# Kernel tuning notes

Hardware: AMD Instinct MI355X
Metric: run time of the kernel (lower is better)

Reference implementation:

```python
import jax, jax.numpy as jnp
import numpy as np

N = 50000      # nodes
E = 500000     # edges
D_IN = 64      # node_in_dim
K = 4          # edge_in_dim
H = 64         # node_hidden_dim
C = 40         # num_class
L = 2          # num_layers


def setup_inputs() -> dict:
    key = jax.random.key(0)
    ks = jax.random.split(key, 10)
    node_features = jax.random.normal(ks[0], (N, D_IN), jnp.float32)
    edge_features = jax.random.normal(ks[1], (L, E, K), jnp.float32)
    src = jax.random.randint(ks[2], (E,), 0, N)
    dst = jax.random.randint(ks[3], (E,), 0, N)
    W0 = jax.random.normal(ks[4], (K * D_IN, H), jnp.float32) * 0.05
    b0 = jnp.zeros((H,), jnp.float32)
    W1 = jax.random.normal(ks[5], (K * H, H), jnp.float32) * 0.05
    b1 = jnp.zeros((H,), jnp.float32)
    Wfc = jax.random.normal(ks[6], (H, C), jnp.float32) * 0.05
    bfc = jnp.zeros((C,), jnp.float32)
    return dict(node_features=node_features, edge_features=edge_features,
                src=src, dst=dst, W0=W0, b0=b0, W1=W1, b1=b1, Wfc=Wfc, bfc=bfc)


def reference(node_features, edge_features, src, dst, W0, b0, W1, b1, Wfc, bfc):
    h = node_features  # [N, d]
    ones = jnp.ones((E,), jnp.float32)
    cnt = jnp.maximum(jax.ops.segment_sum(ones, dst, num_segments=N), 1.0)  # in-degree
    for i, (W, b) in enumerate([(W0, b0), (W1, b1)]):
        e = edge_features[i]          # [E, K]
        hs = h[src]                   # [E, d] edge gather of src node features
        d = hs.shape[1]
        # message: relu(Linear(flatten(e[:,:,None] * h[:,None,:])))
        # flatten order is (K, d), so reshape W -> [K, d, H] and contract directly
        Wr = W.reshape(K, d, H)
        m = jax.nn.relu(jnp.einsum('ek,ed,kdh->eh', e, hs, Wr) + b)  # [E, H]
        s = jax.ops.segment_sum(m, dst, num_segments=N)              # scatter-sum
        h = jax.nn.relu(s / cnt[:, None])                            # mailbox mean + relu
    return h @ Wfc + bfc  # [N, C]
```

## Files before the change

### kernel.cpp

```cpp
#include <hip/hip_runtime.h>
#include <hip/hip_fp16.h>

#define N_NODES 50000
#define N_EDGES 500000
#define DIM 64
#define KDIM 4
#define HID 64
#define NCLS 40
#define NBLK ((N_NODES + 255) / 256)
#define EBLK ((N_EDGES + 255) / 256)

__device__ inline unsigned pack2(float a, float b) {
    __half2 h = __floats2half2_rn(a, b);
    return *(unsigned*)&h;
}
__device__ inline float2 unpack2(unsigned u) {
    __half2 h = *(__half2*)&u;
    return __half22float2(h);
}

__global__ void hist_k(const int* __restrict__ dst, int* __restrict__ cnt) {
    int e = blockIdx.x * 256 + threadIdx.x;
    if (e < N_EDGES) atomicAdd(&cnt[dst[e]], 1);
}

__global__ __launch_bounds__(256) void scan_k(const int* __restrict__ cnt,
                                              int* __restrict__ start,
                                              int* __restrict__ cursor,
                                              volatile int* __restrict__ bflag,
                                              volatile int* __restrict__ bval) {
    __shared__ int ls[256];
    __shared__ int sbase;
    __shared__ int ok_all;
    int b = blockIdx.x, t = threadIdx.x;
    int n = b * 256 + t;
    int v = (n < N_NODES) ? cnt[n] : 0;
    ls[t] = v;
    __syncthreads();
#pragma unroll
    for (int off = 1; off < 256; off <<= 1) {
        int u = (t >= off) ? ls[t - off] : 0;
        __syncthreads();
        ls[t] += u;
        __syncthreads();
    }
    int incl = ls[t];
    int total = ls[255];
    __syncthreads();

    if (t == 0) {
        bval[b] = total;
        __threadfence();
        bflag[b] = 1;
    }

    if (b > 0) {
        for (;;) {
            int f = (t < b) ? bflag[t] : 1;
            if (t == 0) ok_all = 1;
            __syncthreads();
            if (!f) ok_all = 0;
            __syncthreads();
            if (ok_all) break;
        }
        __threadfence();
        int pv = (t < b) ? bval[t] : 0;
        ls[t] = pv;
        __syncthreads();
#pragma unroll
        for (int off = 128; off > 0; off >>= 1) {
            if (t < off) ls[t] += ls[t + off];
            __syncthreads();
        }
        if (t == 0) sbase = ls[0];
        __syncthreads();
    } else {
        if (t == 0) sbase = 0;
        __syncthreads();
    }

    int excl = sbase + incl - v;
    if (n < N_NODES) { start[n] = excl; cursor[n] = excl; }
    if (n == 0) start[N_NODES] = N_EDGES;
}

__global__ void scatter_k(const int* __restrict__ src, const int* __restrict__ dst,
                          const float* __restrict__ ef, int* __restrict__ cursor,
                          uint4* __restrict__ recA) {
    int e = blockIdx.x * 256 + threadIdx.x;
    if (e < N_EDGES) {
        int d = dst[e];
        int pos = atomicAdd(&cursor[d], 1);
        int sn = src[e];
        float4 f0 = ((const float4*)ef)[e];
        recA[pos] = make_uint4((unsigned)sn, pack2(f0.x, f0.y), pack2(f0.z, f0.w), (unsigned)e);
    }
}

__global__ void repack_k(const uint4* __restrict__ recA, const float* __restrict__ ef1,
                         uint4* __restrict__ recB) {
    int i = blockIdx.x * 256 + threadIdx.x;
    if (i < N_EDGES) {
        uint4 r = recA[i];
        int e = (int)r.w;
        float4 f1 = ((const float4*)ef1)[e];
        recB[i] = make_uint4(r.x, pack2(f1.x, f1.y), pack2(f1.z, f1.w), 0u);
    }
}

__global__ __launch_bounds__(256) void transform_k(const float* __restrict__ hin,
                                                   const float* __restrict__ W,
                                                   unsigned* __restrict__ y) {
    __shared__ float sW[2 * 64 * 64];
    __shared__ float sh[64 * 65];
    int t = threadIdx.x;
    int kpair = blockIdx.y;

    const float4* W4 = (const float4*)(W + (size_t)kpair * 2 * 4096);
    float4* sW4 = (float4*)sW;
#pragma unroll
    for (int i = 0; i < 8; ++i) sW4[t + 256 * i] = W4[t + 256 * i];

    int n0 = blockIdx.x * 64;
#pragma unroll
    for (int i = 0; i < 4; ++i) {
        int idx = t + 256 * i;
        int nl = idx >> 4;
        int dg = idx & 15;
        int n = n0 + nl;
        float4 v = make_float4(0.f, 0.f, 0.f, 0.f);
        if (n < N_NODES) v = ((const float4*)hin)[(size_t)n * 16 + dg];
        sh[nl * 65 + dg * 4 + 0] = v.x;
        sh[nl * 65 + dg * 4 + 1] = v.y;
        sh[nl * 65 + dg * 4 + 2] = v.z;
        sh[nl * 65 + dg * 4 + 3] = v.w;
    }
    __syncthreads();

    int nl = t & 31;
    int cg = t >> 5;
    int k_local = cg >> 2;
    int hc0 = (cg & 3) * 16;

    float acc0[16], acc1[16];
#pragma unroll
    for (int j = 0; j < 16; ++j) { acc0[j] = 0.f; acc1[j] = 0.f; }

    for (int d = 0; d < 64; ++d) {
        float a0 = sh[nl * 65 + d];
        float a1 = sh[(nl + 32) * 65 + d];
        const float* wr = &sW[k_local * 4096 + d * 64 + hc0];
#pragma unroll
        for (int j = 0; j < 16; ++j) {
            float w = wr[j];
            acc0[j] = fmaf(a0, w, acc0[j]);
            acc1[j] = fmaf(a1, w, acc1[j]);
        }
    }

    int n_a = n0 + nl, n_b = n0 + nl + 32;
    int cbase = (kpair * 2 + k_local) * 64 + hc0;
    if (n_a < N_NODES) {
        uint4* o = (uint4*)(y + ((size_t)n_a * 256 + cbase) / 2);
        o[0] = make_uint4(pack2(acc0[0], acc0[1]), pack2(acc0[2], acc0[3]),
                          pack2(acc0[4], acc0[5]), pack2(acc0[6], acc0[7]));
        o[1] = make_uint4(pack2(acc0[8], acc0[9]), pack2(acc0[10], acc0[11]),
                          pack2(acc0[12], acc0[13]), pack2(acc0[14], acc0[15]));
    }
    if (n_b < N_NODES) {
        uint4* o = (uint4*)(y + ((size_t)n_b * 256 + cbase) / 2);
        o[0] = make_uint4(pack2(acc1[0], acc1[1]), pack2(acc1[2], acc1[3]),
                          pack2(acc1[4], acc1[5]), pack2(acc1[6], acc1[7]));
        o[1] = make_uint4(pack2(acc1[8], acc1[9]), pack2(acc1[10], acc1[11]),
                          pack2(acc1[12], acc1[13]), pack2(acc1[14], acc1[15]));
    }
}

__device__ inline void load_edge(const uint4 r, const unsigned* __restrict__ y,
                                 int lane, uint2& q0, uint2& q1, uint2& q2, uint2& q3) {
    int sn = (int)r.x;
    const uint2* yb = (const uint2*)(y + (size_t)sn * 128);
    q0 = yb[lane];
    q1 = yb[16 + lane];
    q2 = yb[32 + lane];
    q3 = yb[48 + lane];
}

__device__ inline void compute_edge(const uint4 r, uint2 q0, uint2 q1, uint2 q2, uint2 q3,
                                    const float4 bias, float4& acc) {
    float2 e01 = unpack2(r.y);
    float2 e23 = unpack2(r.z);
    float2 a0 = unpack2(q0.x), a1 = unpack2(q0.y);
    float2 b0 = unpack2(q1.x), b1 = unpack2(q1.y);
    float2 c0 = unpack2(q2.x), c1 = unpack2(q2.y);
    float2 d0 = unpack2(q3.x), d1 = unpack2(q3.y);

    float4 z = bias;
    z.x = fmaf(e01.x, a0.x, z.x); z.y = fmaf(e01.x, a0.y, z.y);
    z.z = fmaf(e01.x, a1.x, z.z); z.w = fmaf(e01.x, a1.y, z.w);
    z.x = fmaf(e01.y, b0.x, z.x); z.y = fmaf(e01.y, b0.y, z.y);
    z.z = fmaf(e01.y, b1.x, z.z); z.w = fmaf(e01.y, b1.y, z.w);
    z.x = fmaf(e23.x, c0.x, z.x); z.y = fmaf(e23.x, c0.y, z.y);
    z.z = fmaf(e23.x, c1.x, z.z); z.w = fmaf(e23.x, c1.y, z.w);
    z.x = fmaf(e23.y, d0.x, z.x); z.y = fmaf(e23.y, d0.y, z.y);
    z.z = fmaf(e23.y, d1.x, z.z); z.w = fmaf(e23.y, d1.y, z.w);

    acc.x += fmaxf(z.x, 0.f);
    acc.y += fmaxf(z.y, 0.f);
    acc.z += fmaxf(z.z, 0.f);
    acc.w += fmaxf(z.w, 0.f);
}

__device__ inline float4 agg_core(const uint4* __restrict__ rec,
                                  const int* __restrict__ start,
                                  const int* __restrict__ cnt,
                                  const unsigned* __restrict__ y,
                                  const float* __restrict__ b,
                                  int g, int lane) {
    int s0 = start[g];
    int deg = cnt[g];
    int s1 = s0 + deg;

    float4 bias = ((const float4*)b)[lane];
    float4 acc = make_float4(0.f, 0.f, 0.f, 0.f);

    int i = s0;
    for (; i + 4 <= s1; i += 4) {
        uint4 r0 = rec[i + 0];
        uint4 r1 = rec[i + 1];
        uint4 r2 = rec[i + 2];
        uint4 r3 = rec[i + 3];
        uint2 a0, a1, a2, a3, b0, b1, b2, b3, c0, c1, c2, c3, d0, d1, d2, d3;
        load_edge(r0, y, lane, a0, a1, a2, a3);
        load_edge(r1, y, lane, b0, b1, b2, b3);
        load_edge(r2, y, lane, c0, c1, c2, c3);
        load_edge(r3, y, lane, d0, d1, d2, d3);
        compute_edge(r0, a0, a1, a2, a3, bias, acc);
        compute_edge(r1, b0, b1, b2, b3, bias, acc);
        compute_edge(r2, c0, c1, c2, c3, bias, acc);
        compute_edge(r3, d0, d1, d2, d3, bias, acc);
    }
    if (i + 2 <= s1) {
        uint4 r0 = rec[i + 0];
        uint4 r1 = rec[i + 1];
        uint2 a0, a1, a2, a3, b0, b1, b2, b3;
        load_edge(r0, y, lane, a0, a1, a2, a3);
        load_edge(r1, y, lane, b0, b1, b2, b3);
        compute_edge(r0, a0, a1, a2, a3, bias, acc);
        compute_edge(r1, b0, b1, b2, b3, bias, acc);
        i += 2;
    }
    if (i < s1) {
        uint4 r0 = rec[i];
        uint2 a0, a1, a2, a3;
        load_edge(r0, y, lane, a0, a1, a2, a3);
        compute_edge(r0, a0, a1, a2, a3, bias, acc);
    }

    float inv = 1.0f / (float)(deg > 1 ? deg : 1);
    float4 r;
    r.x = fmaxf(acc.x * inv, 0.f);
    r.y = fmaxf(acc.y * inv, 0.f);
    r.z = fmaxf(acc.z * inv, 0.f);
    r.w = fmaxf(acc.w * inv, 0.f);
    return r;
}

__global__ __launch_bounds__(256) void agg_k(const uint4* __restrict__ rec,
                                             const int* __restrict__ start,
                                             const int* __restrict__ cnt,
                                             const unsigned* __restrict__ y,
                                             const float* __restrict__ b,
                                             float* __restrict__ hout) {
    int t = blockIdx.x * 256 + threadIdx.x;
    int g = t >> 4;
    int lane = t & 15;
    float4 r = agg_core(rec, start, cnt, y, b, g, lane);
    ((float4*)hout)[(size_t)g * 16 + lane] = r;
}

__global__ __launch_bounds__(256) void agg_fc_k(const uint4* __restrict__ rec,
                                                const int* __restrict__ start,
                                                const int* __restrict__ cnt,
                                                const unsigned* __restrict__ y,
                                                const float* __restrict__ b,
                                                const float* __restrict__ Wfc,
                                                const float* __restrict__ bfc,
                                                float* __restrict__ out) {
    __shared__ float sh_h[16 * 65];
    __shared__ float sWfcT[NCLS * 65];
    __shared__ float sbfc[NCLS];
    int t = threadIdx.x;

    for (int i = t; i < 64 * NCLS; i += 256) {
        int j = i / NCLS;
        int c = i - j * NCLS;
        sWfcT[c * 65 + j] = Wfc[i];
    }
    if (t < NCLS) sbfc[t] = bfc[t];

    int nl = t >> 4;
    int lane = t & 15;
    int g = blockIdx.x * 16 + nl;

    float4 r = agg_core(rec, start, cnt, y, b, g, lane);
    sh_h[nl * 65 + lane * 4 + 0] = r.x;
    sh_h[nl * 65 + lane * 4 + 1] = r.y;
    sh_h[nl * 65 + lane * 4 + 2] = r.z;
    sh_h[nl * 65 + lane * 4 + 3] = r.w;
    __syncthreads();

    for (int item = t; item < 16 * NCLS; item += 256) {
        int rn = item / NCLS;
        int c = item - rn * NCLS;
        float acc = sbfc[c];
        const float* hr = &sh_h[rn * 65];
        const float* wc = &sWfcT[c * 65];
#pragma unroll
        for (int j = 0; j < 64; ++j) acc = fmaf(hr[j], wc[j], acc);
        out[(size_t)(blockIdx.x * 16 + rn) * NCLS + c] = acc;
    }
}

extern "C" void kernel_launch(void* const* d_in, const int* in_sizes, int n_in,
                              void* d_out, int out_size, void* d_ws, size_t ws_size,
                              hipStream_t stream) {
    const float* nf  = (const float*)d_in[0];
    const float* ef  = (const float*)d_in[1];
    const int*   src = (const int*)d_in[2];
    const int*   dst = (const int*)d_in[3];
    const float* W0  = (const float*)d_in[4];
    const float* b0  = (const float*)d_in[5];
    const float* W1  = (const float*)d_in[6];
    const float* b1  = (const float*)d_in[7];
    const float* Wfc = (const float*)d_in[8];
    const float* bfc = (const float*)d_in[9];
    float* out = (float*)d_out;

    char* ws = (char*)d_ws;
    size_t off = 0;
    auto alloc = [&](size_t bytes) -> void* {
        void* p = ws + off;
        off = (off + bytes + 255) & ~(size_t)255;
        return p;
    };
    int*      zbuf   = (int*)     alloc((size_t)(50176 + 512) * 4);
    int*      cnt    = zbuf;
    int*      bflag  = zbuf + 50176;
    int*      bval   = zbuf + 50176 + 256;
    int*      start  = (int*)     alloc((size_t)(N_NODES + 1) * 4);
    int*      cursor = (int*)     alloc((size_t)N_NODES * 4);
    uint4*    recA   = (uint4*)   alloc((size_t)N_EDGES * 16);
    uint4*    recB   = (uint4*)   alloc((size_t)N_EDGES * 16);
    unsigned* y      = (unsigned*)alloc((size_t)N_NODES * 256 * 2);
    float*    hbuf   = (float*)   alloc((size_t)N_NODES * 64 * 4);

    hipMemsetAsync(zbuf, 0, (size_t)(50176 + 512) * 4, stream);

    hist_k<<<EBLK, 256, 0, stream>>>(dst, cnt);
    scan_k<<<NBLK, 256, 0, stream>>>(cnt, start, cursor, bflag, bval);
    scatter_k<<<EBLK, 256, 0, stream>>>(src, dst, ef, cursor, recA);
    repack_k<<<EBLK, 256, 0, stream>>>(recA, ef + (size_t)N_EDGES * 4, recB);

    dim3 tgrid((N_NODES + 63) / 64, 2);
    int agrid = N_NODES / 16;

    transform_k<<<tgrid, 256, 0, stream>>>(nf, W0, y);
    agg_k<<<agrid, 256, 0, stream>>>(recA, start, cnt, y, b0, hbuf);

    transform_k<<<tgrid, 256, 0, stream>>>(hbuf, W1, y);
    agg_fc_k<<<agrid, 256, 0, stream>>>(recB, start, cnt, y, b1, Wfc, bfc, out);
}
```

Before: 306.4 us.

## Sort nodes by in-degree for aggregation balance and use nontemporal record access

Adds a counting-sort pass that builds a permutation of nodes ordered by descending in-degree (capped at 255), and the two aggregation kernels process nodes in that order so that wavefronts hold nodes of similar degree. The aim is to reduce divergence and idle lanes from degree imbalance. Edge record loads and stores now use nontemporal builtins so the streamed records do not evict the gathered node features from cache. It costs three extra small launches and scattered output writes through the permutation.

```diff
diff --git a/kernel.cpp b/kernel.cpp
--- a/kernel.cpp
+++ b/kernel.cpp
@@ -10,6 +10,8 @@
 #define NBLK ((N_NODES + 255) / 256)
 #define EBLK ((N_EDGES + 255) / 256)
 
+typedef unsigned uv4 __attribute__((ext_vector_type(4)));
+
 __device__ inline unsigned pack2(float a, float b) {
     __half2 h = __floats2half2_rn(a, b);
     return *(unsigned*)&h;
@@ -17,6 +19,14 @@
 __device__ inline float2 unpack2(unsigned u) {
     __half2 h = *(__half2*)&u;
     return __half22float2(h);
+}
+__device__ inline uint4 ldnt4(const uint4* p) {
+    uv4 v = __builtin_nontemporal_load((const uv4*)p);
+    return make_uint4(v.x, v.y, v.z, v.w);
+}
+__device__ inline void stnt4(uint4* p, uint4 v) {
+    uv4 w = {v.x, v.y, v.z, v.w};
+    __builtin_nontemporal_store(w, (uv4*)p);
 }
 
 __global__ void hist_k(const int* __restrict__ dst, int* __restrict__ cnt) {
@@ -84,6 +94,41 @@
     if (n == 0) start[N_NODES] = N_EDGES;
 }
 
+__global__ void dhist_k(const int* __restrict__ cnt, int* __restrict__ dbin) {
+    int n = blockIdx.x * 256 + threadIdx.x;
+    if (n < N_NODES) {
+        int d = cnt[n]; if (d > 255) d = 255;
+        atomicAdd(&dbin[255 - d], 1);
+    }
+}
+
+__global__ __launch_bounds__(256) void dscan_k(const int* __restrict__ dbin,
+                                               int* __restrict__ dcursor) {
+    __shared__ int ls[256];
+    int t = threadIdx.x;
+    int v = dbin[t];
+    ls[t] = v;
+    __syncthreads();
+#pragma unroll
+    for (int off = 1; off < 256; off <<= 1) {
+        int u = (t >= off) ? ls[t - off] : 0;
+        __syncthreads();
+        ls[t] += u;
+        __syncthreads();
+    }
+    dcursor[t] = ls[t] - v;
+}
+
+__global__ void dscatter_k(const int* __restrict__ cnt, int* __restrict__ dcursor,
+                           int* __restrict__ perm) {
+    int n = blockIdx.x * 256 + threadIdx.x;
+    if (n < N_NODES) {
+        int d = cnt[n]; if (d > 255) d = 255;
+        int pos = atomicAdd(&dcursor[255 - d], 1);
+        perm[pos] = n;
+    }
+}
+
 __global__ void scatter_k(const int* __restrict__ src, const int* __restrict__ dst,
                           const float* __restrict__ ef, int* __restrict__ cursor,
                           uint4* __restrict__ recA) {
@@ -93,7 +138,7 @@
         int pos = atomicAdd(&cursor[d], 1);
         int sn = src[e];
         float4 f0 = ((const float4*)ef)[e];
-        recA[pos] = make_uint4((unsigned)sn, pack2(f0.x, f0.y), pack2(f0.z, f0.w), (unsigned)e);
+        stnt4(&recA[pos], make_uint4((unsigned)sn, pack2(f0.x, f0.y), pack2(f0.z, f0.w), (unsigned)e));
     }
 }
 
@@ -101,10 +146,10 @@
                          uint4* __restrict__ recB) {
     int i = blockIdx.x * 256 + threadIdx.x;
     if (i < N_EDGES) {
-        uint4 r = recA[i];
+        uint4 r = ldnt4(&recA[i]);
         int e = (int)r.w;
         float4 f1 = ((const float4*)ef1)[e];
-        recB[i] = make_uint4(r.x, pack2(f1.x, f1.y), pack2(f1.z, f1.w), 0u);
+        stnt4(&recB[i], make_uint4(r.x, pack2(f1.x, f1.y), pack2(f1.z, f1.w), 0u));
     }
 }
 
@@ -226,10 +271,10 @@
 
     int i = s0;
     for (; i + 4 <= s1; i += 4) {
-        uint4 r0 = rec[i + 0];
-        uint4 r1 = rec[i + 1];
-        uint4 r2 = rec[i + 2];
-        uint4 r3 = rec[i + 3];
+        uint4 r0 = ldnt4(&rec[i + 0]);
+        uint4 r1 = ldnt4(&rec[i + 1]);
+        uint4 r2 = ldnt4(&rec[i + 2]);
+        uint4 r3 = ldnt4(&rec[i + 3]);
         uint2 a0, a1, a2, a3, b0, b1, b2, b3, c0, c1, c2, c3, d0, d1, d2, d3;
         load_edge(r0, y, lane, a0, a1, a2, a3);
         load_edge(r1, y, lane, b0, b1, b2, b3);
@@ -241,8 +286,8 @@
         compute_edge(r3, d0, d1, d2, d3, bias, acc);
     }
     if (i + 2 <= s1) {
-        uint4 r0 = rec[i + 0];
-        uint4 r1 = rec[i + 1];
+        uint4 r0 = ldnt4(&rec[i + 0]);
+        uint4 r1 = ldnt4(&rec[i + 1]);
         uint2 a0, a1, a2, a3, b0, b1, b2, b3;
         load_edge(r0, y, lane, a0, a1, a2, a3);
         load_edge(r1, y, lane, b0, b1, b2, b3);
@@ -251,7 +296,7 @@
         i += 2;
     }
     if (i < s1) {
-        uint4 r0 = rec[i];
+        uint4 r0 = ldnt4(&rec[i]);
         uint2 a0, a1, a2, a3;
         load_edge(r0, y, lane, a0, a1, a2, a3);
         compute_edge(r0, a0, a1, a2, a3, bias, acc);
@@ -269,12 +314,14 @@
 __global__ __launch_bounds__(256) void agg_k(const uint4* __restrict__ rec,
                                              const int* __restrict__ start,
                                              const int* __restrict__ cnt,
+                                             const int* __restrict__ perm,
                                              const unsigned* __restrict__ y,
                                              const float* __restrict__ b,
                                              float* __restrict__ hout) {
     int t = blockIdx.x * 256 + threadIdx.x;
-    int g = t >> 4;
+    int gid = t >> 4;
     int lane = t & 15;
+    int g = perm[gid];
     float4 r = agg_core(rec, start, cnt, y, b, g, lane);
     ((float4*)hout)[(size_t)g * 16 + lane] = r;
 }
@@ -282,6 +329,7 @@
 __global__ __launch_bounds__(256) void agg_fc_k(const uint4* __restrict__ rec,
                                                 const int* __restrict__ start,
                                                 const int* __restrict__ cnt,
+                                                const int* __restrict__ perm,
                                                 const unsigned* __restrict__ y,
                                                 const float* __restrict__ b,
                                                 const float* __restrict__ Wfc,
@@ -290,6 +338,7 @@
     __shared__ float sh_h[16 * 65];
     __shared__ float sWfcT[NCLS * 65];
     __shared__ float sbfc[NCLS];
+    __shared__ int sgid[16];
     int t = threadIdx.x;
 
     for (int i = t; i < 64 * NCLS; i += 256) {
@@ -301,7 +350,8 @@
 
     int nl = t >> 4;
     int lane = t & 15;
-    int g = blockIdx.x * 16 + nl;
+    int g = perm[blockIdx.x * 16 + nl];
+    if (lane == 0) sgid[nl] = g;
 
     float4 r = agg_core(rec, start, cnt, y, b, g, lane);
     sh_h[nl * 65 + lane * 4 + 0] = r.x;
@@ -318,7 +368,7 @@
         const float* wc = &sWfcT[c * 65];
 #pragma unroll
         for (int j = 0; j < 64; ++j) acc = fmaf(hr[j], wc[j], acc);
-        out[(size_t)(blockIdx.x * 16 + rn) * NCLS + c] = acc;
+        out[(size_t)sgid[rn] * NCLS + c] = acc;
     }
 }
 
@@ -344,21 +394,27 @@
         off = (off + bytes + 255) & ~(size_t)255;
         return p;
     };
-    int*      zbuf   = (int*)     alloc((size_t)(50176 + 512) * 4);
+    int*      zbuf   = (int*)     alloc((size_t)(50176 + 512 + 256) * 4);
     int*      cnt    = zbuf;
     int*      bflag  = zbuf + 50176;
     int*      bval   = zbuf + 50176 + 256;
+    int*      dbin   = zbuf + 50176 + 512;
     int*      start  = (int*)     alloc((size_t)(N_NODES + 1) * 4);
     int*      cursor = (int*)     alloc((size_t)N_NODES * 4);
+    int*      dcur   = (int*)     alloc((size_t)256 * 4);
+    int*      perm   = (int*)     alloc((size_t)N_NODES * 4);
     uint4*    recA   = (uint4*)   alloc((size_t)N_EDGES * 16);
     uint4*    recB   = (uint4*)   alloc((size_t)N_EDGES * 16);
     unsigned* y      = (unsigned*)alloc((size_t)N_NODES * 256 * 2);
     float*    hbuf   = (float*)   alloc((size_t)N_NODES * 64 * 4);
 
-    hipMemsetAsync(zbuf, 0, (size_t)(50176 + 512) * 4, stream);
+    hipMemsetAsync(zbuf, 0, (size_t)(50176 + 512 + 256) * 4, stream);
 
     hist_k<<<EBLK, 256, 0, stream>>>(dst, cnt);
     scan_k<<<NBLK, 256, 0, stream>>>(cnt, start, cursor, bflag, bval);
+    dhist_k<<<NBLK, 256, 0, stream>>>(cnt, dbin);
+    dscan_k<<<1, 256, 0, stream>>>(dbin, dcur);
+    dscatter_k<<<NBLK, 256, 0, stream>>>(cnt, dcur, perm);
     scatter_k<<<EBLK, 256, 0, stream>>>(src, dst, ef, cursor, recA);
     repack_k<<<EBLK, 256, 0, stream>>>(recA, ef + (size_t)N_EDGES * 4, recB);
 
@@ -366,8 +422,8 @@
     int agrid = N_NODES / 16;
 
     transform_k<<<tgrid, 256, 0, stream>>>(nf, W0, y);
-    agg_k<<<agrid, 256, 0, stream>>>(recA, start, cnt, y, b0, hbuf);
+    agg_k<<<agrid, 256, 0, stream>>>(recA, start, cnt, perm, y, b0, hbuf);
 
     transform_k<<<tgrid, 256, 0, stream>>>(hbuf, W1, y);
-    agg_fc_k<<<agrid, 256, 0, stream>>>(recB, start, cnt, y, b1, Wfc, bfc, out);
-}
+    agg_fc_k<<<agrid, 256, 0, stream>>>(recB, start, cnt, perm, y, b1, Wfc, bfc, out);
+}
```

Measured after the change: 641.5 us. +109.3%, slower.

## Interleave transformed features by hidden slice and shard aggregation across four blocks

Applied to the files above, without the earlier changes.

The transform kernel now writes y so that each hidden-column group holds its four k-values contiguously, so each aggregation lane can fetch one uint2 per edge. Aggregation is split into four blocks per 16-node group, one per 16-column slice, which raises parallelism and shrinks the per-edge gather width. The final FC is moved into its own kernel reading an extra h buffer, and edge records are read and written with nontemporal hints. In exchange, the edge records are re-read four times per layer, and the transform block now stages the weights twice.

```diff
diff --git a/kernel.cpp b/kernel.cpp
--- a/kernel.cpp
+++ b/kernel.cpp
@@ -9,6 +9,9 @@
 #define NCLS 40
 #define NBLK ((N_NODES + 255) / 256)
 #define EBLK ((N_EDGES + 255) / 256)
+#define TBLK ((N_NODES + 31) / 32)
+
+typedef unsigned uv4 __attribute__((ext_vector_type(4)));
 
 __device__ inline unsigned pack2(float a, float b) {
     __half2 h = __floats2half2_rn(a, b);
@@ -17,6 +20,14 @@
 __device__ inline float2 unpack2(unsigned u) {
     __half2 h = *(__half2*)&u;
     return __half22float2(h);
+}
+__device__ inline uint4 ldnt4(const uint4* p) {
+    uv4 v = __builtin_nontemporal_load((const uv4*)p);
+    return make_uint4(v.x, v.y, v.z, v.w);
+}
+__device__ inline void stnt4(uint4* p, uint4 v) {
+    uv4 w = {v.x, v.y, v.z, v.w};
+    __builtin_nontemporal_store(w, (uv4*)p);
 }
 
 __global__ void hist_k(const int* __restrict__ dst, int* __restrict__ cnt) {
@@ -93,7 +104,7 @@
         int pos = atomicAdd(&cursor[d], 1);
         int sn = src[e];
         float4 f0 = ((const float4*)ef)[e];
-        recA[pos] = make_uint4((unsigned)sn, pack2(f0.x, f0.y), pack2(f0.z, f0.w), (unsigned)e);
+        stnt4(&recA[pos], make_uint4((unsigned)sn, pack2(f0.x, f0.y), pack2(f0.z, f0.w), (unsigned)e));
     }
 }
 
@@ -101,10 +112,10 @@
                          uint4* __restrict__ recB) {
     int i = blockIdx.x * 256 + threadIdx.x;
     if (i < N_EDGES) {
-        uint4 r = recA[i];
+        uint4 r = ldnt4(&recA[i]);
         int e = (int)r.w;
         float4 f1 = ((const float4*)ef1)[e];
-        recB[i] = make_uint4(r.x, pack2(f1.x, f1.y), pack2(f1.z, f1.w), 0u);
+        stnt4(&recB[i], make_uint4(r.x, pack2(f1.x, f1.y), pack2(f1.z, f1.w), 0u));
     }
 }
 
@@ -112,18 +123,12 @@
                                                    const float* __restrict__ W,
                                                    unsigned* __restrict__ y) {
     __shared__ float sW[2 * 64 * 64];
-    __shared__ float sh[64 * 65];
+    __shared__ float sh[32 * 65];
     int t = threadIdx.x;
-    int kpair = blockIdx.y;
-
-    const float4* W4 = (const float4*)(W + (size_t)kpair * 2 * 4096);
-    float4* sW4 = (float4*)sW;
-#pragma unroll
-    for (int i = 0; i < 8; ++i) sW4[t + 256 * i] = W4[t + 256 * i];
-
-    int n0 = blockIdx.x * 64;
-#pragma unroll
-    for (int i = 0; i < 4; ++i) {
+    int n0 = blockIdx.x * 32;
+
+#pragma unroll
+    for (int i = 0; i < 2; ++i) {
         int idx = t + 256 * i;
         int nl = idx >> 4;
         int dg = idx & 15;
@@ -135,135 +140,132 @@
         sh[nl * 65 + dg * 4 + 2] = v.z;
         sh[nl * 65 + dg * 4 + 3] = v.w;
     }
-    __syncthreads();
 
     int nl = t & 31;
     int cg = t >> 5;
-    int k_local = cg >> 2;
-    int hc0 = (cg & 3) * 16;
-
-    float acc0[16], acc1[16];
-#pragma unroll
-    for (int j = 0; j < 16; ++j) { acc0[j] = 0.f; acc1[j] = 0.f; }
-
-    for (int d = 0; d < 64; ++d) {
-        float a0 = sh[nl * 65 + d];
-        float a1 = sh[(nl + 32) * 65 + d];
-        const float* wr = &sW[k_local * 4096 + d * 64 + hc0];
-#pragma unroll
-        for (int j = 0; j < 16; ++j) {
-            float w = wr[j];
-            acc0[j] = fmaf(a0, w, acc0[j]);
-            acc1[j] = fmaf(a1, w, acc1[j]);
-        }
-    }
-
-    int n_a = n0 + nl, n_b = n0 + nl + 32;
-    int cbase = (kpair * 2 + k_local) * 64 + hc0;
-    if (n_a < N_NODES) {
-        uint4* o = (uint4*)(y + ((size_t)n_a * 256 + cbase) / 2);
-        o[0] = make_uint4(pack2(acc0[0], acc0[1]), pack2(acc0[2], acc0[3]),
-                          pack2(acc0[4], acc0[5]), pack2(acc0[6], acc0[7]));
-        o[1] = make_uint4(pack2(acc0[8], acc0[9]), pack2(acc0[10], acc0[11]),
-                          pack2(acc0[12], acc0[13]), pack2(acc0[14], acc0[15]));
-    }
-    if (n_b < N_NODES) {
-        uint4* o = (uint4*)(y + ((size_t)n_b * 256 + cbase) / 2);
-        o[0] = make_uint4(pack2(acc1[0], acc1[1]), pack2(acc1[2], acc1[3]),
-                          pack2(acc1[4], acc1[5]), pack2(acc1[6], acc1[7]));
-        o[1] = make_uint4(pack2(acc1[8], acc1[9]), pack2(acc1[10], acc1[11]),
-                          pack2(acc1[12], acc1[13]), pack2(acc1[14], acc1[15]));
-    }
-}
-
-__device__ inline void load_edge(const uint4 r, const unsigned* __restrict__ y,
-                                 int lane, uint2& q0, uint2& q1, uint2& q2, uint2& q3) {
-    int sn = (int)r.x;
-    const uint2* yb = (const uint2*)(y + (size_t)sn * 128);
-    q0 = yb[lane];
-    q1 = yb[16 + lane];
-    q2 = yb[32 + lane];
-    q3 = yb[48 + lane];
-}
-
-__device__ inline void compute_edge(const uint4 r, uint2 q0, uint2 q1, uint2 q2, uint2 q3,
-                                    const float4 bias, float4& acc) {
-    float2 e01 = unpack2(r.y);
-    float2 e23 = unpack2(r.z);
-    float2 a0 = unpack2(q0.x), a1 = unpack2(q0.y);
-    float2 b0 = unpack2(q1.x), b1 = unpack2(q1.y);
-    float2 c0 = unpack2(q2.x), c1 = unpack2(q2.y);
-    float2 d0 = unpack2(q3.x), d1 = unpack2(q3.y);
-
-    float4 z = bias;
-    z.x = fmaf(e01.x, a0.x, z.x); z.y = fmaf(e01.x, a0.y, z.y);
-    z.z = fmaf(e01.x, a1.x, z.z); z.w = fmaf(e01.x, a1.y, z.w);
-    z.x = fmaf(e01.y, b0.x, z.x); z.y = fmaf(e01.y, b0.y, z.y);
-    z.z = fmaf(e01.y, b1.x, z.z); z.w = fmaf(e01.y, b1.y, z.w);
-    z.x = fmaf(e23.x, c0.x, z.x); z.y = fmaf(e23.x, c0.y, z.y);
-    z.z = fmaf(e23.x, c1.x, z.z); z.w = fmaf(e23.x, c1.y, z.w);
-    z.x = fmaf(e23.y, d0.x, z.x); z.y = fmaf(e23.y, d0.y, z.y);
-    z.z = fmaf(e23.y, d1.x, z.z); z.w = fmaf(e23.y, d1.y, z.w);
-
-    acc.x += fmaxf(z.x, 0.f);
-    acc.y += fmaxf(z.y, 0.f);
-    acc.z += fmaxf(z.z, 0.f);
-    acc.w += fmaxf(z.w, 0.f);
-}
-
-__device__ inline float4 agg_core(const uint4* __restrict__ rec,
-                                  const int* __restrict__ start,
-                                  const int* __restrict__ cnt,
+    int j0 = cg * 8;
+
+    float accA[8][2];
+    float accB[8][2];
+#pragma unroll
+    for (int c = 0; c < 8; ++c) { accA[c][0] = 0.f; accA[c][1] = 0.f;
+                                  accB[c][0] = 0.f; accB[c][1] = 0.f; }
+
+    {
+        const float4* W4 = (const float4*)W;
+        float4* sW4 = (float4*)sW;
+#pragma unroll
+        for (int i = 0; i < 8; ++i) sW4[t + 256 * i] = W4[t + 256 * i];
+        __syncthreads();
+        for (int d = 0; d < 64; ++d) {
+            float a = sh[nl * 65 + d];
+            const float4* w0 = (const float4*)&sW[d * 64 + j0];
+            const float4* w1 = (const float4*)&sW[4096 + d * 64 + j0];
+            float4 wa0 = w0[0], wb0 = w0[1];
+            float4 wa1 = w1[0], wb1 = w1[1];
+            accA[0][0] = fmaf(a, wa0.x, accA[0][0]); accA[0][1] = fmaf(a, wa1.x, accA[0][1]);
+            accA[1][0] = fmaf(a, wa0.y, accA[1][0]); accA[1][1] = fmaf(a, wa1.y, accA[1][1]);
+            accA[2][0] = fmaf(a, wa0.z, accA[2][0]); accA[2][1] = fmaf(a, wa1.z, accA[2][1]);
+            accA[3][0] = fmaf(a, wa0.w, accA[3][0]); accA[3][1] = fmaf(a, wa1.w, accA[3][1]);
+            accA[4][0] = fmaf(a, wb0.x, accA[4][0]); accA[4][1] = fmaf(a, wb1.x, accA[4][1]);
+            accA[5][0] = fmaf(a, wb0.y, accA[5][0]); accA[5][1] = fmaf(a, wb1.y, accA[5][1]);
+            accA[6][0] = fmaf(a, wb0.z, accA[6][0]); accA[6][1] = fmaf(a, wb1.z, accA[6][1]);
+            accA[7][0] = fmaf(a, wb0.w, accA[7][0]); accA[7][1] = fmaf(a, wb1.w, accA[7][1]);
+        }
+        __syncthreads();
+    }
+    {
+        const float4* W4 = (const float4*)(W + 2 * 4096);
+        float4* sW4 = (float4*)sW;
+#pragma unroll
+        for (int i = 0; i < 8; ++i) sW4[t + 256 * i] = W4[t + 256 * i];
+        __syncthreads();
+        for (int d = 0; d < 64; ++d) {
+            float a = sh[nl * 65 + d];
+            const float4* w0 = (const float4*)&sW[d * 64 + j0];
+            const float4* w1 = (const float4*)&sW[4096 + d * 64 + j0];
+            float4 wa0 = w0[0], wb0 = w0[1];
+            float4 wa1 = w1[0], wb1 = w1[1];
+            accB[0][0] = fmaf(a, wa0.x, accB[0][0]); accB[0][1] = fmaf(a, wa1.x, accB[0][1]);
+            accB[1][0] = fmaf(a, wa0.y, accB[1][0]); accB[1][1] = fmaf(a, wa1.y, accB[1][1]);
+            accB[2][0] = fmaf(a, wa0.z, accB[2][0]); accB[2][1] = fmaf(a, wa1.z, accB[2][1]);
+            accB[3][0] = fmaf(a, wa0.w, accB[3][0]); accB[3][1] = fmaf(a, wa1.w, accB[3][1]);
+            accB[4][0] = fmaf(a, wb0.x, accB[4][0]); accB[4][1] = fmaf(a, wb1.x, accB[4][1]);
+            accB[5][0] = fmaf(a, wb0.y, accB[5][0]); accB[5][1] = fmaf(a, wb1.y, accB[5][1]);
+            accB[6][0] = fmaf(a, wb0.z, accB[6][0]); accB[6][1] = fmaf(a, wb1.z, accB[6][1]);
+            accB[7][0] = fmaf(a, wb0.w, accB[7][0]); accB[7][1] = fmaf(a, wb1.w, accB[7][1]);
+        }
+    }
+
+    int n = n0 + nl;
+    if (n < N_NODES) {
+        int jg = cg >> 1;
+        int jj0 = (cg & 1) * 8;
+        unsigned base = (unsigned)((size_t)0) ;
+        unsigned* yb = y + (size_t)n * 128 + jg * 32 + jj0 * 2;
+        uint4 o0 = make_uint4(pack2(accA[0][0], accA[0][1]), pack2(accB[0][0], accB[0][1]),
+                              pack2(accA[1][0], accA[1][1]), pack2(accB[1][0], accB[1][1]));
+        uint4 o1 = make_uint4(pack2(accA[2][0], accA[2][1]), pack2(accB[2][0], accB[2][1]),
+                              pack2(accA[3][0], accA[3][1]), pack2(accB[3][0], accB[3][1]));
+        uint4 o2 = make_uint4(pack2(accA[4][0], accA[4][1]), pack2(accB[4][0], accB[4][1]),
+                              pack2(accA[5][0], accA[5][1]), pack2(accB[5][0], accB[5][1]));
+        uint4 o3 = make_uint4(pack2(accA[6][0], accA[6][1]), pack2(accB[6][0], accB[6][1]),
+                              pack2(accA[7][0], accA[7][1]), pack2(accB[7][0], accB[7][1]));
+        uint4* o = (uint4*)yb;
+        o[0] = o0; o[1] = o1; o[2] = o2; o[3] = o3;
+        (void)base;
+    }
+}
+
+__device__ inline float agg_shard(const uint4* __restrict__ rec,
+                                  int s0, int deg,
                                   const unsigned* __restrict__ y,
-                                  const float* __restrict__ b,
-                                  int g, int lane) {
-    int s0 = start[g];
-    int deg = cnt[g];
+                                  float bias, int jg, int lane) {
     int s1 = s0 + deg;
-
-    float4 bias = ((const float4*)b)[lane];
-    float4 acc = make_float4(0.f, 0.f, 0.f, 0.f);
-
+    const unsigned* yb = y + jg * 32 + lane * 2;
+    float acc = 0.f;
     int i = s0;
     for (; i + 4 <= s1; i += 4) {
-        uint4 r0 = rec[i + 0];
-        uint4 r1 = rec[i + 1];
-        uint4 r2 = rec[i + 2];
-        uint4 r3 = rec[i + 3];
-        uint2 a0, a1, a2, a3, b0, b1, b2, b3, c0, c1, c2, c3, d0, d1, d2, d3;
-        load_edge(r0, y, lane, a0, a1, a2, a3);
-        load_edge(r1, y, lane, b0, b1, b2, b3);
-        load_edge(r2, y, lane, c0, c1, c2, c3);
-        load_edge(r3, y, lane, d0, d1, d2, d3);
-        compute_edge(r0, a0, a1, a2, a3, bias, acc);
-        compute_edge(r1, b0, b1, b2, b3, bias, acc);
-        compute_edge(r2, c0, c1, c2, c3, bias, acc);
-        compute_edge(r3, d0, d1, d2, d3, bias, acc);
-    }
-    if (i + 2 <= s1) {
-        uint4 r0 = rec[i + 0];
-        uint4 r1 = rec[i + 1];
-        uint2 a0, a1, a2, a3, b0, b1, b2, b3;
-        load_edge(r0, y, lane, a0, a1, a2, a3);
-        load_edge(r1, y, lane, b0, b1, b2, b3);
-        compute_edge(r0, a0, a1, a2, a3, bias, acc);
-        compute_edge(r1, b0, b1, b2, b3, bias, acc);
-        i += 2;
-    }
-    if (i < s1) {
-        uint4 r0 = rec[i];
-        uint2 a0, a1, a2, a3;
-        load_edge(r0, y, lane, a0, a1, a2, a3);
-        compute_edge(r0, a0, a1, a2, a3, bias, acc);
-    }
-
+        uint4 r0 = ldnt4(&rec[i + 0]);
+        uint4 r1 = ldnt4(&rec[i + 1]);
+        uint4 r2 = ldnt4(&rec[i + 2]);
+        uint4 r3 = ldnt4(&rec[i + 3]);
+        uint2 q0 = *(const uint2*)(yb + (size_t)r0.x * 128);
+        uint2 q1 = *(const uint2*)(yb + (size_t)r1.x * 128);
+        uint2 q2 = *(const uint2*)(yb + (size_t)r2.x * 128);
+        uint2 q3 = *(const uint2*)(yb + (size_t)r3.x * 128);
+#pragma unroll
+        for (int u = 0; u < 4; ++u) {
+            uint4 r = (u == 0) ? r0 : (u == 1) ? r1 : (u == 2) ? r2 : r3;
+            uint2 q = (u == 0) ? q0 : (u == 1) ? q1 : (u == 2) ? q2 : q3;
+            float2 e01 = unpack2(r.y);
+            float2 e23 = unpack2(r.z);
+            float2 v01 = unpack2(q.x);
+            float2 v23 = unpack2(q.y);
+            float z = bias;
+            z = fmaf(e01.x, v01.x, z);
+            z = fmaf(e01.y, v01.y, z);
+            z = fmaf(e23.x, v23.x, z);
+            z = fmaf(e23.y, v23.y, z);
+            acc += fmaxf(z, 0.f);
+        }
+    }
+    for (; i < s1; ++i) {
+        uint4 r = ldnt4(&rec[i]);
+        uint2 q = *(const uint2*)(yb + (size_t)r.x * 128);
+        float2 e01 = unpack2(r.y);
+        float2 e23 = unpack2(r.z);
+        float2 v01 = unpack2(q.x);
+        float2 v23 = unpack2(q.y);
+        float z = bias;
+        z = fmaf(e01.x, v01.x, z);
+        z = fmaf(e01.y, v01.y, z);
+        z = fmaf(e23.x, v23.x, z);
+        z = fmaf(e23.y, v23.y, z);
+        acc += fmaxf(z, 0.f);
+    }
     float inv = 1.0f / (float)(deg > 1 ? deg : 1);
-    float4 r;
-    r.x = fmaxf(acc.x * inv, 0.f);
-    r.y = fmaxf(acc.y * inv, 0.f);
-    r.z = fmaxf(acc.z * inv, 0.f);
-    r.w = fmaxf(acc.w * inv, 0.f);
-    return r;
+    return fmaxf(acc * inv, 0.f);
 }
 
 __global__ __launch_bounds__(256) void agg_k(const uint4* __restrict__ rec,
@@ -272,21 +274,20 @@
                                              const unsigned* __restrict__ y,
                                              const float* __restrict__ b,
                                              float* __restrict__ hout) {
-    int t = blockIdx.x * 256 + threadIdx.x;
-    int g = t >> 4;
+    int jg = blockIdx.x & 3;
+    int nb = blockIdx.x >> 2;
+    int t = threadIdx.x;
+    int g = nb * 16 + (t >> 4);
     int lane = t & 15;
-    float4 r = agg_core(rec, start, cnt, y, b, g, lane);
-    ((float4*)hout)[(size_t)g * 16 + lane] = r;
-}
-
-__global__ __launch_bounds__(256) void agg_fc_k(const uint4* __restrict__ rec,
-                                                const int* __restrict__ start,
-                                                const int* __restrict__ cnt,
-                                                const unsigned* __restrict__ y,
-                                                const float* __restrict__ b,
-                                                const float* __restrict__ Wfc,
-                                                const float* __restrict__ bfc,
-                                                float* __restrict__ out) {
+    float bias = b[jg * 16 + lane];
+    float r = agg_shard(rec, start[g], cnt[g], y, bias, jg, lane);
+    hout[(size_t)g * 64 + jg * 16 + lane] = r;
+}
+
+__global__ __launch_bounds__(256) void fc_k(const float* __restrict__ hbuf,
+                                            const float* __restrict__ Wfc,
+                                            const float* __restrict__ bfc,
+                                            float* __restrict__ out) {
     __shared__ float sh_h[16 * 65];
     __shared__ float sWfcT[NCLS * 65];
     __shared__ float sbfc[NCLS];
@@ -300,14 +301,12 @@
     if (t < NCLS) sbfc[t] = bfc[t];
 
     int nl = t >> 4;
-    int lane = t & 15;
-    int g = blockIdx.x * 16 + nl;
-
-    float4 r = agg_core(rec, start, cnt, y, b, g, lane);
-    sh_h[nl * 65 + lane * 4 + 0] = r.x;
-    sh_h[nl * 65 + lane * 4 + 1] = r.y;
-    sh_h[nl * 65 + lane * 4 + 2] = r.z;
-    sh_h[nl * 65 + lane * 4 + 3] = r.w;
+    int dg = t & 15;
+    float4 v = ((const float4*)hbuf)[(size_t)(blockIdx.x * 16 + nl) * 16 + dg];
+    sh_h[nl * 65 + dg * 4 + 0] = v.x;
+    sh_h[nl * 65 + dg * 4 + 1] = v.y;
+    sh_h[nl * 65 + dg * 4 + 2] = v.z;
+    sh_h[nl * 65 + dg * 4 + 3] = v.w;
     __syncthreads();
 
     for (int item = t; item < 16 * NCLS; item += 256) {
@@ -354,6 +353,7 @@
     uint4*    recB   = (uint4*)   alloc((size_t)N_EDGES * 16);
     unsigned* y      = (unsigned*)alloc((size_t)N_NODES * 256 * 2);
     float*    hbuf   = (float*)   alloc((size_t)N_NODES * 64 * 4);
+    float*    hbuf2  = (float*)   alloc((size_t)N_NODES * 64 * 4);
 
     hipMemsetAsync(zbuf, 0, (size_t)(50176 + 512) * 4, stream);
 
@@ -362,12 +362,13 @@
     scatter_k<<<EBLK, 256, 0, stream>>>(src, dst, ef, cursor, recA);
     repack_k<<<EBLK, 256, 0, stream>>>(recA, ef + (size_t)N_EDGES * 4, recB);
 
-    dim3 tgrid((N_NODES + 63) / 64, 2);
-    int agrid = N_NODES / 16;
-
-    transform_k<<<tgrid, 256, 0, stream>>>(nf, W0, y);
+    int agrid = (N_NODES / 16) * 4;
+
+    transform_k<<<TBLK, 256, 0, stream>>>(nf, W0, y);
     agg_k<<<agrid, 256, 0, stream>>>(recA, start, cnt, y, b0, hbuf);
 
-    transform_k<<<tgrid, 256, 0, stream>>>(hbuf, W1, y);
-    agg_fc_k<<<agrid, 256, 0, stream>>>(recB, start, cnt, y, b1, Wfc, bfc, out);
-}
+    transform_k<<<TBLK, 256, 0, stream>>>(hbuf, W1, y);
+    agg_k<<<agrid, 256, 0, stream>>>(recB, start, cnt, y, b1, hbuf2);
+
+    fc_k<<<N_NODES / 16, 256, 0, stream>>>(hbuf2, Wfc, bfc, out);
+}
```

Measured after the change: 422.6 us. 37.9% more time.
